# Kernel tuning notes

Measured on AMD Instinct MI355X. Metric: run time of the kernel, lower is better.

The kernel has to match this reference:

```python
import jax, jax.numpy as jnp
import numpy as np

N = 50000      # nodes
E = 600000     # edges (avg degree 12)
F_IN = 128     # num_features
H = 128        # hidden_feats (== F_IN so both conv layers share weight shapes)
C = 10         # num_classes
L = 2          # num_layers


def setup_inputs() -> dict:
    key = jax.random.key(0)
    ks = jax.random.split(key, 12)
    s = 0.05
    x = jax.random.normal(ks[0], (N, F_IN), dtype=jnp.float32)
    edge_index = jax.random.randint(ks[1], (2, E), 0, N, dtype=jnp.int64)
    # Stacked per-layer TransformerConv params (heads=1): query/key/value/skip linears.
    Wq = jax.random.normal(ks[2], (L, H, F_IN), dtype=jnp.float32) * s
    bq = jax.random.normal(ks[3], (L, H), dtype=jnp.float32) * s
    Wk = jax.random.normal(ks[4], (L, H, F_IN), dtype=jnp.float32) * s
    bk = jax.random.normal(ks[5], (L, H), dtype=jnp.float32) * s
    Wv = jax.random.normal(ks[6], (L, H, F_IN), dtype=jnp.float32) * s
    bv = jax.random.normal(ks[7], (L, H), dtype=jnp.float32) * s
    Ws = jax.random.normal(ks[8], (L, H, F_IN), dtype=jnp.float32) * s
    bs = jax.random.normal(ks[9], (L, H), dtype=jnp.float32) * s
    fc_W = jax.random.normal(ks[10], (C, H), dtype=jnp.float32) * s
    fc_b = jax.random.normal(ks[11], (C,), dtype=jnp.float32) * s
    return {"x": x, "edge_index": edge_index, "Wq": Wq, "bq": bq, "Wk": Wk,
            "bk": bk, "Wv": Wv, "bv": bv, "Ws": Ws, "bs": bs,
            "fc_W": fc_W, "fc_b": fc_b}


def _transformer_conv(h, src, dst, Wq, bq, Wk, bk, Wv, bv, Ws, bs):
    # PyG TransformerConv, heads=1, concat=True, root_weight=True, eval mode.
    d = Wq.shape[0]
    scale = 1.0 / np.sqrt(d).astype(np.float32)
    q = h @ Wq.T + bq          # [N, d]
    k = h @ Wk.T + bk          # [N, d]
    v = h @ Wv.T + bv          # [N, d]
    # per-edge attention score: <q_dst, k_src> / sqrt(d)
    scores = jnp.sum(q[dst] * k[src], axis=-1) * scale   # [E]
    # scatter-softmax over incoming edges of each destination node
    m = jax.ops.segment_max(scores, dst, num_segments=N)           # [N]
    e = jnp.exp(scores - m[dst])                                   # [E]
    denom = jax.ops.segment_sum(e, dst, num_segments=N)            # [N]
    alpha = e / denom[dst]                                         # [E]
    agg = jax.ops.segment_sum(alpha[:, None] * v[src], dst, num_segments=N)  # [N, d]
    return agg + (h @ Ws.T + bs)  # root/skip connection


def reference(x, edge_index, Wq, bq, Wk, bk, Wv, bv, Ws, bs, fc_W, fc_b):
    src = edge_index[0]
    dst = edge_index[1]
    h = x
    for l in range(L):  # fixed small layer loop
        h = _transformer_conv(h, src, dst, Wq[l], bq[l], Wk[l], bk[l],
                              Wv[l], bv[l], Ws[l], bs[l])
        h = jax.nn.relu(h)  # dropout is identity in eval mode
    logits = h @ fc_W.T + fc_b  # [N, C]
    return jax.nn.log_softmax(logits, axis=1)
```

## Files before the change

### kernel.cpp

```cpp
#include <hip/hip_runtime.h>
#include <math.h>

#define N_NODES 50000
#define N_EDGES 600000
#define DIM 128
#define NCLS 10
#define MTILES 391
#define CHUNKS_PER_TILE 2048
#define NB_SCAN 49
#define XB_CHUNKS (N_NODES * DIM / 8)

typedef _Float16 h2 __attribute__((ext_vector_type(2)));
typedef _Float16 half8 __attribute__((ext_vector_type(8)));
typedef __attribute__((ext_vector_type(4))) float f32x4;

__device__ inline h2 pkh(float a, float b) {
    auto r = __builtin_amdgcn_cvt_pkrtz(a, b);
    return *(h2*)&r;
}
__device__ inline unsigned h2u(h2 v) { return *(unsigned*)&v; }
__device__ inline h2 u2h(unsigned u) { return *(h2*)&u; }

__device__ inline float dot2acc(h2 a, h2 b, float c) {
#if __has_builtin(__builtin_amdgcn_fdot2)
    return __builtin_amdgcn_fdot2(a, b, c, false);
#else
    return fmaf((float)a.x, (float)b.x, fmaf((float)a.y, (float)b.y, c));
#endif
}

__global__ void deg_kernel(const int* __restrict__ dst, int* __restrict__ deg) {
    int e = blockIdx.x * blockDim.x + threadIdx.x;
    if (e < N_EDGES) atomicAdd(&deg[dst[e]], 1);
}

__global__ __launch_bounds__(1024) void scan1_kernel(
        const int* __restrict__ deg, int* __restrict__ row_start,
        int* __restrict__ partials) {
    __shared__ int buf[1024];
    int b = blockIdx.x, t = threadIdx.x;
    int i = b * 1024 + t;
    buf[t] = (i < N_NODES) ? deg[i] : 0;
    __syncthreads();
    for (int off = 1; off < 1024; off <<= 1) {
        int tv = (t >= off) ? buf[t - off] : 0;
        __syncthreads();
        buf[t] += tv;
        __syncthreads();
    }
    if (i < N_NODES) row_start[i + 1] = buf[t];
    if (t == 1023) partials[b] = buf[1023];
}

__global__ void scan2_kernel(const int* __restrict__ partials, int* __restrict__ blockoff) {
    int l = threadIdx.x;
    int v = (l < NB_SCAN) ? partials[l] : 0;
    int inc = v;
    #pragma unroll
    for (int off = 1; off < 64; off <<= 1) {
        int t = __shfl_up(inc, off);
        if (l >= off) inc += t;
    }
    if (l < NB_SCAN) blockoff[l] = inc - v;
}

__global__ __launch_bounds__(1024) void scan3_kernel(
        const int* __restrict__ blockoff, int* __restrict__ row_start,
        int* __restrict__ cursor) {
    int b = blockIdx.x, t = threadIdx.x;
    int i = b * 1024 + t;
    if (i < N_NODES) {
        int val = row_start[i + 1] + blockoff[b];
        row_start[i + 1] = val;
        if (i + 1 < N_NODES) cursor[i + 1] = val;
    }
    if (i == 0) { row_start[0] = 0; cursor[0] = 0; }
}

__global__ void fill_kernel(const int* __restrict__ src, const int* __restrict__ dst,
                            int* __restrict__ cursor, int* __restrict__ col) {
    int e = blockIdx.x * blockDim.x + threadIdx.x;
    if (e < N_EDGES) {
        int pos = atomicAdd(&cursor[dst[e]], 1);
        col[pos] = src[e];
    }
}

__global__ __launch_bounds__(256) void convert_kernel(
        const float* __restrict__ x,
        const float* __restrict__ Wq, const float* __restrict__ Wk,
        const float* __restrict__ Wv, const float* __restrict__ Ws,
        unsigned short* __restrict__ xh, unsigned short* __restrict__ wfrag) {
    int b = blockIdx.x;
    if (b < 8) {
        int l = b >> 2, m = b & 3;
        const float* W = (m == 0 ? Wq : m == 1 ? Wk : m == 2 ? Wv : Ws) + l * DIM * DIM;
        unsigned short* out = wfrag + (size_t)b * (CHUNKS_PER_TILE * 8);
        for (int i = threadIdx.x; i < CHUNKS_PER_TILE; i += 256) {
            int tile = i >> 6, lane = i & 63;
            int row = (tile >> 2) * 16 + (lane & 15);
            int k0 = (tile & 3) * 32 + (lane >> 4) * 8;
            const float4* p = (const float4*)(W + row * DIM + k0);
            float4 a = p[0], bb = p[1];
            uint4 o;
            o.x = h2u(pkh(a.x, a.y));  o.y = h2u(pkh(a.z, a.w));
            o.z = h2u(pkh(bb.x, bb.y)); o.w = h2u(pkh(bb.z, bb.w));
            *(uint4*)(out + (size_t)i * 8) = o;
        }
    } else {
        int i = (b - 8) * 256 + threadIdx.x;
        if (i >= XB_CHUNKS) return;
        const float4* p = (const float4*)(x + (size_t)i * 8);
        float4 a = p[0], bb = p[1];
        uint4 o;
        o.x = h2u(pkh(a.x, a.y));  o.y = h2u(pkh(a.z, a.w));
        o.z = h2u(pkh(bb.x, bb.y)); o.w = h2u(pkh(bb.z, bb.w));
        *(uint4*)(xh + (size_t)i * 8) = o;
    }
}

__global__ __launch_bounds__(512) void linear_kernel(
        const unsigned short* __restrict__ hb,
        const unsigned short* __restrict__ wfrag,
        const float* __restrict__ bq, const float* __restrict__ bk,
        const float* __restrict__ bv, const float* __restrict__ bs,
        unsigned short* __restrict__ Qb, unsigned short* __restrict__ Kb,
        unsigned short* __restrict__ Vb, unsigned short* __restrict__ Sb) {
    __shared__ unsigned short hs[16384];
    __shared__ unsigned short wsm[16384];
    int tid = threadIdx.x;
    int tile = blockIdx.x;
    uint4* lh = (uint4*)hs;
    uint4* lw = (uint4*)wsm;
    #pragma unroll
    for (int j = 0; j < 4; ++j) {
        int i = tid + j * 512;
        int s = i >> 6, lane = i & 63;
        int row = tile * 128 + ((s >> 2) << 4) + (lane & 15);
        int k0 = ((s & 3) << 5) + ((lane >> 4) << 3);
        row = row < N_NODES ? row : N_NODES - 1;
        lh[i] = *(const uint4*)(hb + (size_t)row * DIM + k0);
    }
    int wave = tid >> 6, lane = tid & 63;
    int node = tile * 128 + wave * 16 + (lane & 15);
    int cq = (lane >> 4) * 4;

    for (int m = 0; m < 4; ++m) {
        const uint4* gw = (const uint4*)(wfrag + (size_t)m * (CHUNKS_PER_TILE * 8));
        __syncthreads();
        #pragma unroll
        for (int j = 0; j < 4; ++j) lw[tid + j * 512] = gw[tid + j * 512];
        __syncthreads();

        f32x4 acc[8];
        #pragma unroll
        for (int nt = 0; nt < 8; ++nt) acc[nt] = (f32x4){0.f, 0.f, 0.f, 0.f};
        #pragma unroll
        for (int ks = 0; ks < 4; ++ks) {
            half8 hbv = *(const half8*)(lh + (wave * 4 + ks) * 64 + lane);
            #pragma unroll
            for (int nt = 0; nt < 8; ++nt)
                acc[nt] = __builtin_amdgcn_mfma_f32_16x16x32_f16(
                              *(const half8*)(lw + (nt * 4 + ks) * 64 + lane),
                              hbv, acc[nt], 0, 0, 0);
        }

        const float* bias = (m == 0 ? bq : m == 1 ? bk : m == 2 ? bv : bs);
        unsigned short* out = (m == 0 ? Qb : m == 1 ? Kb : m == 2 ? Vb : Sb);
        if (node < N_NODES) {
            #pragma unroll
            for (int nt = 0; nt < 8; ++nt) {
                int colv = nt * 16 + cq;
                float4 bi = *(const float4*)(bias + colv);
                uint2 o;
                o.x = h2u(pkh(acc[nt][0] + bi.x, acc[nt][1] + bi.y));
                o.y = h2u(pkh(acc[nt][2] + bi.z, acc[nt][3] + bi.w));
                *(uint2*)(out + (size_t)node * DIM + colv) = o;
            }
        }
    }
}

__global__ __launch_bounds__(256) void attn_kernel(
        const unsigned short* __restrict__ Qb, const unsigned short* __restrict__ Kb,
        const unsigned short* __restrict__ Vb, const unsigned short* __restrict__ Sb,
        const int* __restrict__ row_start, const int* __restrict__ col,
        unsigned short* __restrict__ hout) {
    int wave = threadIdx.x >> 6;
    int lane = threadIdx.x & 63;
    int g = lane >> 4, gl = lane & 15;
    int n = blockIdx.x * 4 + wave;
    if (n >= N_NODES) return;

    const char* Kc = (const char*)Kb;
    const char* Vc = (const char*)Vb;
    const float qs = 0.08838834764831843f * 1.4426950408889634f;
    uint4 qu = *(const uint4*)((const char*)Qb + (((unsigned)n) << 8) + (gl << 4));
    h2 q0 = u2h(qu.x), q1 = u2h(qu.y), q2 = u2h(qu.z), q3 = u2h(qu.w);

    int e0 = row_start[n], e1 = row_start[n + 1];
    int eq_end = e0 + ((e1 - e0) & ~3);
    const float NEG = -1.0e30f;
    float m = NEG, den = 0.f;
    h2 a0 = (h2)0, a1 = (h2)0, a2 = (h2)0, a3 = (h2)0;

    int e = e0 + g;
    for (; e < eq_end; e += 4) {
        int s = col[e];
        unsigned off = (((unsigned)s) << 8) + (gl << 4);
        uint4 kv = *(const uint4*)(Kc + off);
        uint4 vv = *(const uint4*)(Vc + off);
        float p = dot2acc(u2h(kv.x), q0, 0.f);
        p = dot2acc(u2h(kv.y), q1, p);
        p = dot2acc(u2h(kv.z), q2, p);
        p = dot2acc(u2h(kv.w), q3, p);
        p += __shfl_xor(p, 1);
        p += __shfl_xor(p, 2);
        p += __shfl_xor(p, 4);
        p += __shfl_xor(p, 8);
        p *= qs;
        float nm = fmaxf(m, p);
        float fac = exp2f(m - nm);
        float w = exp2f(p - nm);
        den = fmaf(den, fac, w);
        h2 fw = pkh(fac, w);
        h2 fac2 = { fw.x, fw.x };
        h2 w2 = { fw.y, fw.y };
        a0 = a0 * fac2 + w2 * u2h(vv.x);
        a1 = a1 * fac2 + w2 * u2h(vv.y);
        a2 = a2 * fac2 + w2 * u2h(vv.z);
        a3 = a3 * fac2 + w2 * u2h(vv.w);
        m = nm;
    }
    if (e < e1) {
        int s = col[e];
        unsigned off = (((unsigned)s) << 8) + (gl << 4);
        uint4 kv = *(const uint4*)(Kc + off);
        uint4 vv = *(const uint4*)(Vc + off);
        float p = dot2acc(u2h(kv.x), q0, 0.f);
        p = dot2acc(u2h(kv.y), q1, p);
        p = dot2acc(u2h(kv.z), q2, p);
        p = dot2acc(u2h(kv.w), q3, p);
        p += __shfl_xor(p, 1);
        p += __shfl_xor(p, 2);
        p += __shfl_xor(p, 4);
        p += __shfl_xor(p, 8);
        p *= qs;
        float nm = fmaxf(m, p);
        float fac = exp2f(m - nm);
        float w = exp2f(p - nm);
        den = fmaf(den, fac, w);
        h2 fw = pkh(fac, w);
        h2 fac2 = { fw.x, fw.x };
        h2 w2 = { fw.y, fw.y };
        a0 = a0 * fac2 + w2 * u2h(vv.x);
        a1 = a1 * fac2 + w2 * u2h(vv.y);
        a2 = a2 * fac2 + w2 * u2h(vv.z);
        a3 = a3 * fac2 + w2 * u2h(vv.w);
        m = nm;
    }

    float acc[8];
    acc[0] = (float)a0.x; acc[1] = (float)a0.y;
    acc[2] = (float)a1.x; acc[3] = (float)a1.y;
    acc[4] = (float)a2.x; acc[5] = (float)a2.y;
    acc[6] = (float)a3.x; acc[7] = (float)a3.y;
    float M = m;
    M = fmaxf(M, __shfl_xor(M, 16));
    M = fmaxf(M, __shfl_xor(M, 32));
    float fac = exp2f(m - M);
    float d = den * fac;
    d += __shfl_xor(d, 16);
    d += __shfl_xor(d, 32);
    #pragma unroll
    for (int j = 0; j < 8; ++j) {
        float a = acc[j] * fac;
        a += __shfl_xor(a, 16);
        a += __shfl_xor(a, 32);
        acc[j] = a;
    }
    float inv = (d > 0.f) ? 1.f / d : 0.f;

    uint4 su = *(const uint4*)((const char*)Sb + (((unsigned)n) << 8) + (gl << 4));
    if (g == 0) {
        h2 s0 = u2h(su.x), s1 = u2h(su.y), s2 = u2h(su.z), s3 = u2h(su.w);
        uint4 o;
        o.x = h2u(pkh(fmaxf(fmaf(acc[0], inv, (float)s0.x), 0.f),
                      fmaxf(fmaf(acc[1], inv, (float)s0.y), 0.f)));
        o.y = h2u(pkh(fmaxf(fmaf(acc[2], inv, (float)s1.x), 0.f),
                      fmaxf(fmaf(acc[3], inv, (float)s1.y), 0.f)));
        o.z = h2u(pkh(fmaxf(fmaf(acc[4], inv, (float)s2.x), 0.f),
                      fmaxf(fmaf(acc[5], inv, (float)s2.y), 0.f)));
        o.w = h2u(pkh(fmaxf(fmaf(acc[6], inv, (float)s3.x), 0.f),
                      fmaxf(fmaf(acc[7], inv, (float)s3.y), 0.f)));
        *(uint4*)((char*)hout + (((unsigned)n) << 8) + (gl << 4)) = o;
    }
}

__global__ __launch_bounds__(256) void logits_kernel(
        const unsigned short* __restrict__ hb, const float* __restrict__ fcW,
        const float* __restrict__ fcb, float* __restrict__ out) {
    int wave = threadIdx.x >> 6, lane = threadIdx.x & 63;
    int n = blockIdx.x * 4 + wave;
    if (n >= N_NODES) return;
    unsigned hu = ((const unsigned*)hb)[(size_t)n * 64 + lane];
    h2 hh = u2h(hu);
    float hx = (float)hh.x, hy = (float)hh.y;
    float logit[NCLS];
    #pragma unroll
    for (int c = 0; c < NCLS; ++c) {
        float2 w = ((const float2*)(fcW + c * DIM))[lane];
        float p = hx * w.x + hy * w.y;
        #pragma unroll
        for (int off = 32; off >= 1; off >>= 1) p += __shfl_xor(p, off);
        logit[c] = p + fcb[c];
    }
    float mx = logit[0];
    #pragma unroll
    for (int c = 1; c < NCLS; ++c) mx = fmaxf(mx, logit[c]);
    float se = 0.f;
    #pragma unroll
    for (int c = 0; c < NCLS; ++c) se += __expf(logit[c] - mx);
    float lse = mx + logf(se);
    if (lane < NCLS) {
        float myv = 0.f;
        #pragma unroll
        for (int c = 0; c < NCLS; ++c) if (lane == c) myv = logit[c];
        out[(size_t)n * NCLS + lane] = myv - lse;
    }
}

extern "C" void kernel_launch(void* const* d_in, const int* in_sizes, int n_in,
                              void* d_out, int out_size, void* d_ws, size_t ws_size,
                              hipStream_t stream) {
    const float* x   = (const float*)d_in[0];
    const int*   ei  = (const int*)d_in[1];
    const float* Wq  = (const float*)d_in[2];
    const float* bq  = (const float*)d_in[3];
    const float* Wk  = (const float*)d_in[4];
    const float* bk  = (const float*)d_in[5];
    const float* Wv  = (const float*)d_in[6];
    const float* bv  = (const float*)d_in[7];
    const float* Ws  = (const float*)d_in[8];
    const float* bs  = (const float*)d_in[9];
    const float* fcW = (const float*)d_in[10];
    const float* fcb = (const float*)d_in[11];
    const int* src = ei;
    const int* dst = ei + N_EDGES;

    size_t NF = (size_t)N_NODES * DIM;
    unsigned short* Qb = (unsigned short*)d_ws;
    unsigned short* Kb = Qb + NF;
    unsigned short* Vb = Kb + NF;
    unsigned short* Sb = Vb + NF;
    unsigned short* h1 = Sb + NF;
    unsigned short* xh = h1 + NF;
    unsigned short* wfrag = xh + NF;
    int* ints      = (int*)(wfrag + 8 * CHUNKS_PER_TILE * 8);
    int* row_start = ints;
    int* cursor    = row_start + N_NODES + 1;
    int* col       = cursor + N_NODES;
    int* partials  = col + N_EDGES;
    int* blockoff  = partials + 64;

    (void)hipMemsetAsync(cursor, 0, N_NODES * sizeof(int), stream);
    deg_kernel<<<(N_EDGES + 255) / 256, 256, 0, stream>>>(dst, cursor);
    scan1_kernel<<<NB_SCAN, 1024, 0, stream>>>(cursor, row_start, partials);
    scan2_kernel<<<1, 64, 0, stream>>>(partials, blockoff);
    scan3_kernel<<<NB_SCAN, 1024, 0, stream>>>(blockoff, row_start, cursor);
    fill_kernel<<<(N_EDGES + 255) / 256, 256, 0, stream>>>(src, dst, cursor, col);

    convert_kernel<<<8 + (XB_CHUNKS + 255) / 256, 256, 0, stream>>>(
        x, Wq, Wk, Wv, Ws, xh, wfrag);

    const int AGRID = (N_NODES + 3) / 4;

    linear_kernel<<<MTILES, 512, 0, stream>>>(xh, wfrag, bq, bk, bv, bs, Qb, Kb, Vb, Sb);
    attn_kernel<<<AGRID, 256, 0, stream>>>(Qb, Kb, Vb, Sb, row_start, col, h1);
    linear_kernel<<<MTILES, 512, 0, stream>>>(h1, wfrag + 4 * CHUNKS_PER_TILE * 8,
                                              bq + DIM, bk + DIM, bv + DIM, bs + DIM,
                                              Qb, Kb, Vb, Sb);
    attn_kernel<<<AGRID, 256, 0, stream>>>(Qb, Kb, Vb, Sb, row_start, col, xh);
    logits_kernel<<<AGRID, 256, 0, stream>>>(xh, fcW, fcb, (float*)d_out);
}
```

Baseline: 271.3 us.

## Prefetch neighbor K/V in attention, fuse x conversion and scan stages

The attention kernel now software-pipelines its gather loop. It loads the next edge's column index and K/V rows while computing the current edge, and uses a clamped, masked tail instead of a separate remainder path. The fp32-to-fp16 conversion of x moves into the first linear kernel through a template flag, which removes a separate pass and buffer over x. The scan2 kernel is folded into scan3: each block sums the partials of the blocks before it, which saves a launch. In exchange, the masked tail can do some wasted loads, and register pressure rises from holding prefetched data.

```diff
diff --git a/kernel.cpp b/kernel.cpp
--- a/kernel.cpp
+++ b/kernel.cpp
@@ -8,7 +8,6 @@
 #define MTILES 391
 #define CHUNKS_PER_TILE 2048
 #define NB_SCAN 49
-#define XB_CHUNKS (N_NODES * DIM / 8)
 
 typedef _Float16 h2 __attribute__((ext_vector_type(2)));
 typedef _Float16 half8 __attribute__((ext_vector_type(8)));
@@ -52,25 +51,22 @@
     if (t == 1023) partials[b] = buf[1023];
 }
 
-__global__ void scan2_kernel(const int* __restrict__ partials, int* __restrict__ blockoff) {
-    int l = threadIdx.x;
-    int v = (l < NB_SCAN) ? partials[l] : 0;
-    int inc = v;
-    #pragma unroll
-    for (int off = 1; off < 64; off <<= 1) {
-        int t = __shfl_up(inc, off);
-        if (l >= off) inc += t;
-    }
-    if (l < NB_SCAN) blockoff[l] = inc - v;
-}
-
 __global__ __launch_bounds__(1024) void scan3_kernel(
-        const int* __restrict__ blockoff, int* __restrict__ row_start,
+        const int* __restrict__ partials, int* __restrict__ row_start,
         int* __restrict__ cursor) {
+    __shared__ int boff_s;
     int b = blockIdx.x, t = threadIdx.x;
+    if (t < 64) {
+        int v = (t < b) ? partials[t] : 0;
+        #pragma unroll
+        for (int off = 32; off >= 1; off >>= 1) v += __shfl_xor(v, off);
+        if (t == 0) boff_s = v;
+    }
+    __syncthreads();
+    int boff = boff_s;
     int i = b * 1024 + t;
     if (i < N_NODES) {
-        int val = row_start[i + 1] + blockoff[b];
+        int val = row_start[i + 1] + boff;
         row_start[i + 1] = val;
         if (i + 1 < N_NODES) cursor[i + 1] = val;
     }
@@ -86,41 +82,30 @@
     }
 }
 
-__global__ __launch_bounds__(256) void convert_kernel(
-        const float* __restrict__ x,
+__global__ __launch_bounds__(256) void convertw_kernel(
         const float* __restrict__ Wq, const float* __restrict__ Wk,
         const float* __restrict__ Wv, const float* __restrict__ Ws,
-        unsigned short* __restrict__ xh, unsigned short* __restrict__ wfrag) {
+        unsigned short* __restrict__ wfrag) {
     int b = blockIdx.x;
-    if (b < 8) {
-        int l = b >> 2, m = b & 3;
-        const float* W = (m == 0 ? Wq : m == 1 ? Wk : m == 2 ? Wv : Ws) + l * DIM * DIM;
-        unsigned short* out = wfrag + (size_t)b * (CHUNKS_PER_TILE * 8);
-        for (int i = threadIdx.x; i < CHUNKS_PER_TILE; i += 256) {
-            int tile = i >> 6, lane = i & 63;
-            int row = (tile >> 2) * 16 + (lane & 15);
-            int k0 = (tile & 3) * 32 + (lane >> 4) * 8;
-            const float4* p = (const float4*)(W + row * DIM + k0);
-            float4 a = p[0], bb = p[1];
-            uint4 o;
-            o.x = h2u(pkh(a.x, a.y));  o.y = h2u(pkh(a.z, a.w));
-            o.z = h2u(pkh(bb.x, bb.y)); o.w = h2u(pkh(bb.z, bb.w));
-            *(uint4*)(out + (size_t)i * 8) = o;
-        }
-    } else {
-        int i = (b - 8) * 256 + threadIdx.x;
-        if (i >= XB_CHUNKS) return;
-        const float4* p = (const float4*)(x + (size_t)i * 8);
+    int l = b >> 2, m = b & 3;
+    const float* W = (m == 0 ? Wq : m == 1 ? Wk : m == 2 ? Wv : Ws) + l * DIM * DIM;
+    unsigned short* out = wfrag + (size_t)b * (CHUNKS_PER_TILE * 8);
+    for (int i = threadIdx.x; i < CHUNKS_PER_TILE; i += 256) {
+        int tile = i >> 6, lane = i & 63;
+        int row = (tile >> 2) * 16 + (lane & 15);
+        int k0 = (tile & 3) * 32 + (lane >> 4) * 8;
+        const float4* p = (const float4*)(W + row * DIM + k0);
         float4 a = p[0], bb = p[1];
         uint4 o;
         o.x = h2u(pkh(a.x, a.y));  o.y = h2u(pkh(a.z, a.w));
         o.z = h2u(pkh(bb.x, bb.y)); o.w = h2u(pkh(bb.z, bb.w));
-        *(uint4*)(xh + (size_t)i * 8) = o;
-    }
-}
-
+        *(uint4*)(out + (size_t)i * 8) = o;
+    }
+}
+
+template <bool F32IN>
 __global__ __launch_bounds__(512) void linear_kernel(
-        const unsigned short* __restrict__ hb,
+        const void* __restrict__ hb_,
         const unsigned short* __restrict__ wfrag,
         const float* __restrict__ bq, const float* __restrict__ bk,
         const float* __restrict__ bv, const float* __restrict__ bs,
@@ -139,7 +124,18 @@
         int row = tile * 128 + ((s >> 2) << 4) + (lane & 15);
         int k0 = ((s & 3) << 5) + ((lane >> 4) << 3);
         row = row < N_NODES ? row : N_NODES - 1;
-        lh[i] = *(const uint4*)(hb + (size_t)row * DIM + k0);
+        if (F32IN) {
+            const float* hf = (const float*)hb_;
+            const float4* p = (const float4*)(hf + (size_t)row * DIM + k0);
+            float4 a = p[0], bb = p[1];
+            uint4 o;
+            o.x = h2u(pkh(a.x, a.y));  o.y = h2u(pkh(a.z, a.w));
+            o.z = h2u(pkh(bb.x, bb.y)); o.w = h2u(pkh(bb.z, bb.w));
+            lh[i] = o;
+        } else {
+            const unsigned short* hh = (const unsigned short*)hb_;
+            lh[i] = *(const uint4*)(hh + (size_t)row * DIM + k0);
+        }
     }
     int wave = tid >> 6, lane = tid & 63;
     int node = tile * 128 + wave * 16 + (lane & 15);
@@ -192,72 +188,61 @@
     int n = blockIdx.x * 4 + wave;
     if (n >= N_NODES) return;
 
-    const char* Kc = (const char*)Kb;
-    const char* Vc = (const char*)Vb;
+    const char* Kc = (const char*)Kb + (gl << 4);
+    const char* Vc = (const char*)Vb + (gl << 4);
     const float qs = 0.08838834764831843f * 1.4426950408889634f;
     uint4 qu = *(const uint4*)((const char*)Qb + (((unsigned)n) << 8) + (gl << 4));
     h2 q0 = u2h(qu.x), q1 = u2h(qu.y), q2 = u2h(qu.z), q3 = u2h(qu.w);
 
     int e0 = row_start[n], e1 = row_start[n + 1];
-    int eq_end = e0 + ((e1 - e0) & ~3);
+    int deg = e1 - e0;
     const float NEG = -1.0e30f;
     float m = NEG, den = 0.f;
     h2 a0 = (h2)0, a1 = (h2)0, a2 = (h2)0, a3 = (h2)0;
 
-    int e = e0 + g;
-    for (; e < eq_end; e += 4) {
-        int s = col[e];
-        unsigned off = (((unsigned)s) << 8) + (gl << 4);
+    if (deg > 0) {
+        int last = e1 - 1;
+        int e = e0 + g;
+        int c0 = e < last ? e : last;
+        int s = col[c0];
+        unsigned off = ((unsigned)s) << 8;
         uint4 kv = *(const uint4*)(Kc + off);
         uint4 vv = *(const uint4*)(Vc + off);
-        float p = dot2acc(u2h(kv.x), q0, 0.f);
-        p = dot2acc(u2h(kv.y), q1, p);
-        p = dot2acc(u2h(kv.z), q2, p);
-        p = dot2acc(u2h(kv.w), q3, p);
-        p += __shfl_xor(p, 1);
-        p += __shfl_xor(p, 2);
-        p += __shfl_xor(p, 4);
-        p += __shfl_xor(p, 8);
-        p *= qs;
-        float nm = fmaxf(m, p);
-        float fac = exp2f(m - nm);
-        float w = exp2f(p - nm);
-        den = fmaf(den, fac, w);
-        h2 fw = pkh(fac, w);
-        h2 fac2 = { fw.x, fw.x };
-        h2 w2 = { fw.y, fw.y };
-        a0 = a0 * fac2 + w2 * u2h(vv.x);
-        a1 = a1 * fac2 + w2 * u2h(vv.y);
-        a2 = a2 * fac2 + w2 * u2h(vv.z);
-        a3 = a3 * fac2 + w2 * u2h(vv.w);
-        m = nm;
-    }
-    if (e < e1) {
-        int s = col[e];
-        unsigned off = (((unsigned)s) << 8) + (gl << 4);
-        uint4 kv = *(const uint4*)(Kc + off);
-        uint4 vv = *(const uint4*)(Vc + off);
-        float p = dot2acc(u2h(kv.x), q0, 0.f);
-        p = dot2acc(u2h(kv.y), q1, p);
-        p = dot2acc(u2h(kv.z), q2, p);
-        p = dot2acc(u2h(kv.w), q3, p);
-        p += __shfl_xor(p, 1);
-        p += __shfl_xor(p, 2);
-        p += __shfl_xor(p, 4);
-        p += __shfl_xor(p, 8);
-        p *= qs;
-        float nm = fmaxf(m, p);
-        float fac = exp2f(m - nm);
-        float w = exp2f(p - nm);
-        den = fmaf(den, fac, w);
-        h2 fw = pkh(fac, w);
-        h2 fac2 = { fw.x, fw.x };
-        h2 w2 = { fw.y, fw.y };
-        a0 = a0 * fac2 + w2 * u2h(vv.x);
-        a1 = a1 * fac2 + w2 * u2h(vv.y);
-        a2 = a2 * fac2 + w2 * u2h(vv.z);
-        a3 = a3 * fac2 + w2 * u2h(vv.w);
-        m = nm;
+        int en = e + 4;
+        int c1 = en < last ? en : last;
+        int sn = col[c1];
+        int T = (deg + 3) >> 2;
+        for (int t = 0; t < T; ++t) {
+            bool valid = e < e1;
+            uint4 kvc = kv, vvc = vv;
+            unsigned offn = ((unsigned)sn) << 8;
+            kv = *(const uint4*)(Kc + offn);
+            vv = *(const uint4*)(Vc + offn);
+            e = en; en = e + 4;
+            int c2 = en < last ? en : last;
+            sn = col[c2];
+            float p = dot2acc(u2h(kvc.x), q0, 0.f);
+            p = dot2acc(u2h(kvc.y), q1, p);
+            p = dot2acc(u2h(kvc.z), q2, p);
+            p = dot2acc(u2h(kvc.w), q3, p);
+            p += __shfl_xor(p, 1);
+            p += __shfl_xor(p, 2);
+            p += __shfl_xor(p, 4);
+            p += __shfl_xor(p, 8);
+            p = valid ? p * qs : NEG;
+            float nm = fmaxf(m, p);
+            float fac = exp2f(m - nm);
+            float w = valid ? exp2f(p - nm) : 0.f;
+            den = fmaf(den, fac, w);
+            h2 fw = pkh(fac, w);
+            h2 fac2 = { fw.x, fw.x };
+            h2 w2 = { fw.y, fw.y };
+            a0 = a0 * fac2 + w2 * u2h(vvc.x);
+            a1 = a1 * fac2 + w2 * u2h(vvc.y);
+            a2 = a2 * fac2 + w2 * u2h(vvc.z);
+            a3 = a3 * fac2 + w2 * u2h(vvc.w);
+            m = nm;
+        }
     }
 
     float acc[8];
@@ -354,32 +339,29 @@
     unsigned short* Vb = Kb + NF;
     unsigned short* Sb = Vb + NF;
     unsigned short* h1 = Sb + NF;
-    unsigned short* xh = h1 + NF;
-    unsigned short* wfrag = xh + NF;
+    unsigned short* wfrag = h1 + NF;
     int* ints      = (int*)(wfrag + 8 * CHUNKS_PER_TILE * 8);
     int* row_start = ints;
     int* cursor    = row_start + N_NODES + 1;
     int* col       = cursor + N_NODES;
     int* partials  = col + N_EDGES;
-    int* blockoff  = partials + 64;
 
     (void)hipMemsetAsync(cursor, 0, N_NODES * sizeof(int), stream);
     deg_kernel<<<(N_EDGES + 255) / 256, 256, 0, stream>>>(dst, cursor);
     scan1_kernel<<<NB_SCAN, 1024, 0, stream>>>(cursor, row_start, partials);
-    scan2_kernel<<<1, 64, 0, stream>>>(partials, blockoff);
-    scan3_kernel<<<NB_SCAN, 1024, 0, stream>>>(blockoff, row_start, cursor);
+    scan3_kernel<<<NB_SCAN, 1024, 0, stream>>>(partials, row_start, cursor);
     fill_kernel<<<(N_EDGES + 255) / 256, 256, 0, stream>>>(src, dst, cursor, col);
 
-    convert_kernel<<<8 + (XB_CHUNKS + 255) / 256, 256, 0, stream>>>(
-        x, Wq, Wk, Wv, Ws, xh, wfrag);
+    convertw_kernel<<<8, 256, 0, stream>>>(Wq, Wk, Wv, Ws, wfrag);
 
     const int AGRID = (N_NODES + 3) / 4;
 
-    linear_kernel<<<MTILES, 512, 0, stream>>>(xh, wfrag, bq, bk, bv, bs, Qb, Kb, Vb, Sb);
+    linear_kernel<true><<<MTILES, 512, 0, stream>>>(x, wfrag, bq, bk, bv, bs,
+                                                    Qb, Kb, Vb, Sb);
     attn_kernel<<<AGRID, 256, 0, stream>>>(Qb, Kb, Vb, Sb, row_start, col, h1);
-    linear_kernel<<<MTILES, 512, 0, stream>>>(h1, wfrag + 4 * CHUNKS_PER_TILE * 8,
-                                              bq + DIM, bk + DIM, bv + DIM, bs + DIM,
-                                              Qb, Kb, Vb, Sb);
-    attn_kernel<<<AGRID, 256, 0, stream>>>(Qb, Kb, Vb, Sb, row_start, col, xh);
-    logits_kernel<<<AGRID, 256, 0, stream>>>(xh, fcW, fcb, (float*)d_out);
-}
+    linear_kernel<false><<<MTILES, 512, 0, stream>>>(h1, wfrag + 4 * CHUNKS_PER_TILE * 8,
+                                                     bq + DIM, bk + DIM, bv + DIM, bs + DIM,
+                                                     Qb, Kb, Vb, Sb);
+    attn_kernel<<<AGRID, 256, 0, stream>>>(Qb, Kb, Vb, Sb, row_start, col, h1);
+    logits_kernel<<<AGRID, 256, 0, stream>>>(h1, fcW, fcb, (float*)d_out);
+}
```

Measured after the change: 269.7 us. Within noise of the previous version (-0.6%).
